# Optimization experiments

Measured on AMD Instinct MI355X. Metric: run time of the kernel, lower is better.

## Reference

```python
import jax, jax.numpy as jnp
import numpy as np

N_NODES = 100000
HIDDEN = 64
N_EDGES = 1600000


def _sage_conv(x, edge_index, Wl, Wr, b):
    # PyG SAGEConv (mean aggr): out_i = W_l @ mean_{j->i} x_j + W_r @ x_i + b
    src, dst = edge_index[0], edge_index[1]
    msg = x[src]                                      # [E, H] gather
    agg = jax.ops.segment_sum(msg, dst, num_segments=N_NODES)  # [N, H]
    deg = jax.ops.segment_sum(jnp.ones((msg.shape[0],), x.dtype), dst,
                              num_segments=N_NODES)
    agg = agg / jnp.maximum(deg, 1.0)[:, None]
    return agg @ Wl.T + x @ Wr.T + b


def setup_inputs() -> dict:
    key = jax.random.key(0)
    ks = jax.random.split(key, 8)
    s = 1.0 / np.sqrt(HIDDEN)
    return {
        "emb": jax.random.normal(ks[0], (N_NODES, HIDDEN), jnp.float32),
        "Wl1": jax.random.normal(ks[1], (HIDDEN, HIDDEN), jnp.float32) * s,
        "Wr1": jax.random.normal(ks[2], (HIDDEN, HIDDEN), jnp.float32) * s,
        "b1": jnp.zeros((HIDDEN,), jnp.float32),
        "Wl2": jax.random.normal(ks[3], (HIDDEN, HIDDEN), jnp.float32) * s,
        "Wr2": jax.random.normal(ks[4], (HIDDEN, HIDDEN), jnp.float32) * s,
        "b2": jnp.zeros((HIDDEN,), jnp.float32),
        "node_id": jnp.arange(N_NODES, dtype=jnp.int64 if jax.config.jax_enable_x64 else jnp.int32),
        "edge_index": jax.random.randint(ks[5], (2, N_EDGES), 0, N_NODES),
    }


def reference(emb, Wl1, Wr1, b1, Wl2, Wr2, b2, node_id, edge_index):
    # Embedding lookup
    x = emb[node_id]                                   # [N, H]
    # GNN: relu(conv1) -> conv2
    x = jax.nn.relu(_sage_conv(x, edge_index, Wl1, Wr1, b1))
    x = _sage_conv(x, edge_index, Wl2, Wr2, b2)
    # Classifier: per-edge dot product of endpoint features
    ef1 = x[edge_index[0]]                             # [E, H]
    ef2 = x[edge_index[1]]                             # [E, H]
    return (ef1 * ef2).sum(axis=-1)                    # [E]
```

## Files before the change

kernel.cpp:

```cpp
#include <hip/hip_runtime.h>

#define N_NODES 100000
#define HID 64
#define N_EDGES 1600000
#define NB 391
#define C_EPB 6400

typedef __attribute__((ext_vector_type(8))) short bf16x8;
typedef __attribute__((ext_vector_type(4))) float f32x4;

__device__ __forceinline__ unsigned short f2bf(float f) {
    unsigned u = __float_as_uint(f);
    u = (u + 0x7FFFu + ((u >> 16) & 1u)) >> 16;
    return (unsigned short)u;
}
__device__ __forceinline__ float bf2f(unsigned short h) {
    return __uint_as_float(((unsigned)h) << 16);
}
__device__ __forceinline__ float bflo(unsigned w) { return __uint_as_float(w << 16); }
__device__ __forceinline__ float bfhi(unsigned w) { return __uint_as_float(w & 0xFFFF0000u); }

__global__ void gather_bf16_kernel(const float* __restrict__ emb,
                                   const int* __restrict__ nid,
                                   unsigned short* __restrict__ xh) {
    int i = blockIdx.x * blockDim.x + threadIdx.x;
    const int total = N_NODES * (HID / 4);
    if (i >= total) return;
    int row = i >> 4;
    int c   = i & 15;
    int s   = nid[row];
    float4 v = reinterpret_cast<const float4*>(emb)[(size_t)s * 16 + c];
    uint2 p;
    p.x = (unsigned)f2bf(v.x) | ((unsigned)f2bf(v.y) << 16);
    p.y = (unsigned)f2bf(v.z) | ((unsigned)f2bf(v.w) << 16);
    reinterpret_cast<uint2*>(xh)[(size_t)row * 16 + c] = p;
}

__global__ void bucket_hist(const int* __restrict__ dst,
                            int* __restrict__ bhist) {
    __shared__ int h[NB];
    for (int i = threadIdx.x; i < NB; i += blockDim.x) h[i] = 0;
    __syncthreads();
    int nt = gridDim.x * blockDim.x;
    const int4* d4 = (const int4*)dst;
    for (int q = blockIdx.x * blockDim.x + threadIdx.x; q < N_EDGES / 4; q += nt) {
        int4 v = d4[q];
        atomicAdd(&h[v.x >> 8], 1);
        atomicAdd(&h[v.y >> 8], 1);
        atomicAdd(&h[v.z >> 8], 1);
        atomicAdd(&h[v.w >> 8], 1);
    }
    __syncthreads();
    for (int i = threadIdx.x; i < NB; i += blockDim.x)
        if (h[i]) atomicAdd(&bhist[i], h[i]);
}

__global__ void bucket_scan(const int* __restrict__ bhist,
                            int* __restrict__ boff,
                            int* __restrict__ bcursor) {
    __shared__ int s[512];
    int v = (threadIdx.x < NB) ? bhist[threadIdx.x] : 0;
    s[threadIdx.x] = v;
    __syncthreads();
    for (int off = 1; off < 512; off <<= 1) {
        int t = (threadIdx.x >= off) ? s[threadIdx.x - off] : 0;
        __syncthreads();
        s[threadIdx.x] += t;
        __syncthreads();
    }
    if (threadIdx.x < NB) {
        int ex = s[threadIdx.x] - v;
        boff[threadIdx.x] = ex;
        bcursor[threadIdx.x] = ex;
    }
}

__global__ void bucket_scatter(const int* __restrict__ src,
                               const int* __restrict__ dst,
                               int* __restrict__ bcursor,
                               int2* __restrict__ pairs) {
    __shared__ int h[NB];
    __shared__ int base[NB];
    for (int i = threadIdx.x; i < NB; i += blockDim.x) h[i] = 0;
    __syncthreads();
    int e0 = blockIdx.x * C_EPB;
    int e1 = e0 + C_EPB; if (e1 > N_EDGES) e1 = N_EDGES;
    for (int e = e0 + threadIdx.x; e < e1; e += blockDim.x)
        atomicAdd(&h[dst[e] >> 8], 1);
    __syncthreads();
    for (int i = threadIdx.x; i < NB; i += blockDim.x) {
        int c = h[i];
        base[i] = c ? atomicAdd(&bcursor[i], c) : 0;
    }
    __syncthreads();
    for (int i = threadIdx.x; i < NB; i += blockDim.x) h[i] = 0;
    __syncthreads();
    for (int e = e0 + threadIdx.x; e < e1; e += blockDim.x) {
        int d = dst[e];
        int b = d >> 8;
        int slot = base[b] + atomicAdd(&h[b], 1);
        pairs[slot] = make_int2(src[e], d);
    }
}

__global__ void bucket_csr(const int2* __restrict__ pairs,
                           const int* __restrict__ boff,
                           const int* __restrict__ bcursor,
                           int* __restrict__ row_start,
                           int* __restrict__ adj) {
    __shared__ int cnt[256];
    __shared__ int sc[256];
    int b = blockIdx.x;
    int node0 = b << 8;
    int p0 = boff[b];
    int p1 = bcursor[b];
    int t = threadIdx.x;
    cnt[t] = 0;
    __syncthreads();
    for (int p = p0 + t; p < p1; p += 256)
        atomicAdd(&cnt[pairs[p].y & 255], 1);
    __syncthreads();
    int v = cnt[t];
    sc[t] = v;
    __syncthreads();
    for (int off = 1; off < 256; off <<= 1) {
        int u = (t >= off) ? sc[t - off] : 0;
        __syncthreads();
        sc[t] += u;
        __syncthreads();
    }
    sc[t] = p0 + sc[t] - v;
    __syncthreads();
    int node = node0 + t;
    if (node <= N_NODES) row_start[node] = sc[t];
    __syncthreads();
    for (int p = p0 + t; p < p1; p += 256) {
        int2 pr = pairs[p];
        int slot = atomicAdd(&sc[pr.y & 255], 1);
        adj[slot] = pr.x;
    }
}

__global__ void agg_kernel(const int* __restrict__ row_start,
                           const int* __restrict__ adj,
                           const unsigned short* __restrict__ xh,
                           unsigned short* __restrict__ M) {
    int lane = threadIdx.x & 63;
    int slot = lane >> 4;
    int c    = lane & 15;
    int wpb = blockDim.x >> 6;
    int wid = blockIdx.x * wpb + (threadIdx.x >> 6);
    int stride = gridDim.x * wpb;
    const uint2* xw = (const uint2*)xh;
    uint2* Mw = (uint2*)M;
    for (int row = wid; row < N_NODES; row += stride) {
        int beg = row_start[row], end = row_start[row + 1];
        float a0 = 0.f, a1 = 0.f, a2 = 0.f, a3 = 0.f;
        int j = beg + slot;
        for (; j + 12 < end; j += 16) {
            int s0 = adj[j], s1 = adj[j + 4], s2 = adj[j + 8], s3 = adj[j + 12];
            uint2 v0 = xw[(size_t)s0 * 16 + c];
            uint2 v1 = xw[(size_t)s1 * 16 + c];
            uint2 v2 = xw[(size_t)s2 * 16 + c];
            uint2 v3 = xw[(size_t)s3 * 16 + c];
            a0 += bflo(v0.x) + bflo(v1.x) + bflo(v2.x) + bflo(v3.x);
            a1 += bfhi(v0.x) + bfhi(v1.x) + bfhi(v2.x) + bfhi(v3.x);
            a2 += bflo(v0.y) + bflo(v1.y) + bflo(v2.y) + bflo(v3.y);
            a3 += bfhi(v0.y) + bfhi(v1.y) + bfhi(v2.y) + bfhi(v3.y);
        }
        for (; j < end; j += 4) {
            uint2 v = xw[(size_t)adj[j] * 16 + c];
            a0 += bflo(v.x); a1 += bfhi(v.x);
            a2 += bflo(v.y); a3 += bfhi(v.y);
        }
        a0 += __shfl_xor(a0, 16); a0 += __shfl_xor(a0, 32);
        a1 += __shfl_xor(a1, 16); a1 += __shfl_xor(a1, 32);
        a2 += __shfl_xor(a2, 16); a2 += __shfl_xor(a2, 32);
        a3 += __shfl_xor(a3, 16); a3 += __shfl_xor(a3, 32);
        if (slot == 0) {
            float inv = 1.0f / fmaxf((float)(end - beg), 1.0f);
            uint2 p;
            p.x = (unsigned)f2bf(a0 * inv) | ((unsigned)f2bf(a1 * inv) << 16);
            p.y = (unsigned)f2bf(a2 * inv) | ((unsigned)f2bf(a3 * inv) << 16);
            Mw[(size_t)row * 16 + c] = p;
        }
    }
}

__global__ void gemm_kernel(const unsigned short* __restrict__ Am,
                            const unsigned short* __restrict__ As,
                            const float* __restrict__ Wl,
                            const float* __restrict__ Wr,
                            const float* __restrict__ bias,
                            unsigned short* __restrict__ H,
                            int relu) {
    int lane = threadIdx.x & 63;
    int m = lane & 15, quad = lane >> 4;

    bf16x8 wf[2][2][4];
    for (int mat = 0; mat < 2; ++mat) {
        const float* W = mat ? Wr : Wl;
        for (int ks = 0; ks < 2; ++ks)
            for (int ct = 0; ct < 4; ++ct) {
                const float* p = W + (ct * 16 + m) * HID + ks * 32 + quad * 8;
                bf16x8 f;
                #pragma unroll
                for (int j = 0; j < 8; ++j) f[j] = (short)f2bf(p[j]);
                wf[mat][ks][ct] = f;
            }
    }
    float bv[4];
    #pragma unroll
    for (int ct = 0; ct < 4; ++ct) bv[ct] = bias[ct * 16 + m];

    int wpb = blockDim.x >> 6;
    int wid = blockIdx.x * wpb + (threadIdx.x >> 6);
    int stride = gridDim.x * wpb;
    const int NT = N_NODES / 16;
    for (int t = wid; t < NT; t += stride) {
        f32x4 acc[4] = {{0,0,0,0},{0,0,0,0},{0,0,0,0},{0,0,0,0}};
        size_t rowbase = ((size_t)t * 16 + m) * HID;
        #pragma unroll
        for (int ks = 0; ks < 2; ++ks) {
            bf16x8 a0 = *(const bf16x8*)(Am + rowbase + ks * 32 + quad * 8);
            bf16x8 a1 = *(const bf16x8*)(As + rowbase + ks * 32 + quad * 8);
            #pragma unroll
            for (int ct = 0; ct < 4; ++ct) {
                acc[ct] = __builtin_amdgcn_mfma_f32_16x16x32_bf16(a0, wf[0][ks][ct], acc[ct], 0, 0, 0);
                acc[ct] = __builtin_amdgcn_mfma_f32_16x16x32_bf16(a1, wf[1][ks][ct], acc[ct], 0, 0, 0);
            }
        }
        #pragma unroll
        for (int ct = 0; ct < 4; ++ct) {
            #pragma unroll
            for (int r = 0; r < 4; ++r) {
                float v = acc[ct][r] + bv[ct];
                if (relu) v = fmaxf(v, 0.f);
                H[((size_t)t * 16 + quad * 4 + r) * HID + ct * 16 + m] = f2bf(v);
            }
        }
    }
}

__global__ void edge_dot_kernel(const int* __restrict__ src,
                                const int* __restrict__ dst,
                                const unsigned short* __restrict__ h,
                                float* __restrict__ out) {
    int t = blockIdx.x * blockDim.x + threadIdx.x;
    int g = t >> 3;
    int c = t & 7;
    int e0 = g * 2;
    if (e0 >= N_EDGES) return;
    int a0 = src[e0],     b0 = dst[e0];
    int a1 = src[e0 + 1], b1 = dst[e0 + 1];
    const uint4* h4 = reinterpret_cast<const uint4*>(h);
    uint4 va0 = h4[(size_t)a0 * 8 + c];
    uint4 vb0 = h4[(size_t)b0 * 8 + c];
    uint4 va1 = h4[(size_t)a1 * 8 + c];
    uint4 vb1 = h4[(size_t)b1 * 8 + c];
    float p0 = bflo(va0.x) * bflo(vb0.x) + bfhi(va0.x) * bfhi(vb0.x)
             + bflo(va0.y) * bflo(vb0.y) + bfhi(va0.y) * bfhi(vb0.y)
             + bflo(va0.z) * bflo(vb0.z) + bfhi(va0.z) * bfhi(vb0.z)
             + bflo(va0.w) * bflo(vb0.w) + bfhi(va0.w) * bfhi(vb0.w);
    float p1 = bflo(va1.x) * bflo(vb1.x) + bfhi(va1.x) * bfhi(vb1.x)
             + bflo(va1.y) * bflo(vb1.y) + bfhi(va1.y) * bfhi(vb1.y)
             + bflo(va1.z) * bflo(vb1.z) + bfhi(va1.z) * bfhi(vb1.z)
             + bflo(va1.w) * bflo(vb1.w) + bfhi(va1.w) * bfhi(vb1.w);
    p0 += __shfl_xor(p0, 1); p0 += __shfl_xor(p0, 2); p0 += __shfl_xor(p0, 4);
    p1 += __shfl_xor(p1, 1); p1 += __shfl_xor(p1, 2); p1 += __shfl_xor(p1, 4);
    if (c == 0) reinterpret_cast<float2*>(out)[g] = make_float2(p0, p1);
}

extern "C" void kernel_launch(void* const* d_in, const int* in_sizes, int n_in,
                              void* d_out, int out_size, void* d_ws, size_t ws_size,
                              hipStream_t stream) {
    const float* emb = (const float*)d_in[0];
    const float* Wl1 = (const float*)d_in[1];
    const float* Wr1 = (const float*)d_in[2];
    const float* b1  = (const float*)d_in[3];
    const float* Wl2 = (const float*)d_in[4];
    const float* Wr2 = (const float*)d_in[5];
    const float* b2  = (const float*)d_in[6];
    const int*   nid = (const int*)d_in[7];
    const int*   ei  = (const int*)d_in[8];
    const int* esrc = ei;
    const int* edst = ei + N_EDGES;
    float* out = (float*)d_out;

    const size_t NH = (size_t)N_NODES * HID;
    unsigned short* xh  = (unsigned short*)d_ws;
    unsigned short* h1h = xh + NH;
    unsigned short* h2h = h1h + NH;
    unsigned short* M   = h2h + NH;
    int* ib        = (int*)(M + NH);
    int* row_start = ib;
    int* adj       = ib + N_NODES + 64;
    int2* pairs    = (int2*)(adj + N_EDGES + 64);
    int* bhist     = (int*)(pairs + N_EDGES);
    int* boff      = bhist + NB + 1;
    int* bcursor   = boff + NB + 1;

    hipMemsetAsync(bhist, 0, NB * sizeof(int), stream);

    gather_bf16_kernel<<<(N_NODES * 16 + 255) / 256, 256, 0, stream>>>(emb, nid, xh);

    bucket_hist<<<256, 256, 0, stream>>>(edst, bhist);
    bucket_scan<<<1, 512, 0, stream>>>(bhist, boff, bcursor);
    bucket_scatter<<<(N_EDGES + C_EPB - 1) / C_EPB, 256, 0, stream>>>(esrc, edst, bcursor, pairs);
    bucket_csr<<<NB, 256, 0, stream>>>(pairs, boff, bcursor, row_start, adj);

    agg_kernel<<<2048, 256, 0, stream>>>(row_start, adj, xh, M);
    gemm_kernel<<<512, 256, 0, stream>>>(M, xh, Wl1, Wr1, b1, h1h, 1);

    agg_kernel<<<2048, 256, 0, stream>>>(row_start, adj, h1h, M);
    gemm_kernel<<<512, 256, 0, stream>>>(M, h1h, Wl2, Wr2, b2, h2h, 0);

    edge_dot_kernel<<<((size_t)(N_EDGES / 2) * 8 + 255) / 256, 256, 0, stream>>>(esrc, edst, h2h, out);
}
```

Measured before the change: 302.4 us.

## Compute edge dot products in CSR order and fuse gather with histogram

The edge-dot classifier now walks the destination-sorted CSR. Each destination row is loaded once and reused across all its incoming edges, and results are scattered to their original edge positions through a new eord array built during CSR construction. The embedding gather and the bucket histogram are merged into one launch to drop a kernel launch. The costs are an extra 6.4 MB index array with its writes, scattered 4-byte output stores, and edge ids packed into 24 bits of the pair word.

```diff
diff --git a/kernel.cpp b/kernel.cpp
--- a/kernel.cpp
+++ b/kernel.cpp
@@ -5,6 +5,7 @@
 #define N_EDGES 1600000
 #define NB 391
 #define C_EPB 6400
+#define GATHER_BLOCKS 6250
 
 typedef __attribute__((ext_vector_type(8))) short bf16x8;
 typedef __attribute__((ext_vector_type(4))) float f32x4;
@@ -20,30 +21,32 @@
 __device__ __forceinline__ float bflo(unsigned w) { return __uint_as_float(w << 16); }
 __device__ __forceinline__ float bfhi(unsigned w) { return __uint_as_float(w & 0xFFFF0000u); }
 
-__global__ void gather_bf16_kernel(const float* __restrict__ emb,
+__global__ void gather_hist_kernel(const float* __restrict__ emb,
                                    const int* __restrict__ nid,
-                                   unsigned short* __restrict__ xh) {
-    int i = blockIdx.x * blockDim.x + threadIdx.x;
-    const int total = N_NODES * (HID / 4);
-    if (i >= total) return;
-    int row = i >> 4;
-    int c   = i & 15;
-    int s   = nid[row];
-    float4 v = reinterpret_cast<const float4*>(emb)[(size_t)s * 16 + c];
-    uint2 p;
-    p.x = (unsigned)f2bf(v.x) | ((unsigned)f2bf(v.y) << 16);
-    p.y = (unsigned)f2bf(v.z) | ((unsigned)f2bf(v.w) << 16);
-    reinterpret_cast<uint2*>(xh)[(size_t)row * 16 + c] = p;
-}
-
-__global__ void bucket_hist(const int* __restrict__ dst,
-                            int* __restrict__ bhist) {
+                                   unsigned short* __restrict__ xh,
+                                   const int* __restrict__ dst,
+                                   int* __restrict__ bhist) {
+    if (blockIdx.x < GATHER_BLOCKS) {
+        int i = blockIdx.x * blockDim.x + threadIdx.x;
+        const int total = N_NODES * (HID / 4);
+        if (i >= total) return;
+        int row = i >> 4;
+        int c   = i & 15;
+        int s   = nid[row];
+        float4 v = reinterpret_cast<const float4*>(emb)[(size_t)s * 16 + c];
+        uint2 p;
+        p.x = (unsigned)f2bf(v.x) | ((unsigned)f2bf(v.y) << 16);
+        p.y = (unsigned)f2bf(v.z) | ((unsigned)f2bf(v.w) << 16);
+        reinterpret_cast<uint2*>(xh)[(size_t)row * 16 + c] = p;
+        return;
+    }
     __shared__ int h[NB];
     for (int i = threadIdx.x; i < NB; i += blockDim.x) h[i] = 0;
     __syncthreads();
-    int nt = gridDim.x * blockDim.x;
+    int hb = blockIdx.x - GATHER_BLOCKS;
+    const int nt = 256 * 256;
     const int4* d4 = (const int4*)dst;
-    for (int q = blockIdx.x * blockDim.x + threadIdx.x; q < N_EDGES / 4; q += nt) {
+    for (int q = hb * blockDim.x + threadIdx.x; q < N_EDGES / 4; q += nt) {
         int4 v = d4[q];
         atomicAdd(&h[v.x >> 8], 1);
         atomicAdd(&h[v.y >> 8], 1);
@@ -99,7 +102,7 @@
         int d = dst[e];
         int b = d >> 8;
         int slot = base[b] + atomicAdd(&h[b], 1);
-        pairs[slot] = make_int2(src[e], d);
+        pairs[slot] = make_int2(src[e], (d & 255) | (e << 8));
     }
 }
 
@@ -107,7 +110,8 @@
                            const int* __restrict__ boff,
                            const int* __restrict__ bcursor,
                            int* __restrict__ row_start,
-                           int* __restrict__ adj) {
+                           int* __restrict__ adj,
+                           int* __restrict__ eord) {
     __shared__ int cnt[256];
     __shared__ int sc[256];
     int b = blockIdx.x;
@@ -138,6 +142,7 @@
         int2 pr = pairs[p];
         int slot = atomicAdd(&sc[pr.y & 255], 1);
         adj[slot] = pr.x;
+        eord[slot] = (int)(((unsigned)pr.y) >> 8);
     }
 }
 
@@ -242,33 +247,52 @@
     }
 }
 
-__global__ void edge_dot_kernel(const int* __restrict__ src,
-                                const int* __restrict__ dst,
-                                const unsigned short* __restrict__ h,
-                                float* __restrict__ out) {
-    int t = blockIdx.x * blockDim.x + threadIdx.x;
-    int g = t >> 3;
-    int c = t & 7;
-    int e0 = g * 2;
-    if (e0 >= N_EDGES) return;
-    int a0 = src[e0],     b0 = dst[e0];
-    int a1 = src[e0 + 1], b1 = dst[e0 + 1];
-    const uint4* h4 = reinterpret_cast<const uint4*>(h);
-    uint4 va0 = h4[(size_t)a0 * 8 + c];
-    uint4 vb0 = h4[(size_t)b0 * 8 + c];
-    uint4 va1 = h4[(size_t)a1 * 8 + c];
-    uint4 vb1 = h4[(size_t)b1 * 8 + c];
-    float p0 = bflo(va0.x) * bflo(vb0.x) + bfhi(va0.x) * bfhi(vb0.x)
-             + bflo(va0.y) * bflo(vb0.y) + bfhi(va0.y) * bfhi(vb0.y)
-             + bflo(va0.z) * bflo(vb0.z) + bfhi(va0.z) * bfhi(vb0.z)
-             + bflo(va0.w) * bflo(vb0.w) + bfhi(va0.w) * bfhi(vb0.w);
-    float p1 = bflo(va1.x) * bflo(vb1.x) + bfhi(va1.x) * bfhi(vb1.x)
-             + bflo(va1.y) * bflo(vb1.y) + bfhi(va1.y) * bfhi(vb1.y)
-             + bflo(va1.z) * bflo(vb1.z) + bfhi(va1.z) * bfhi(vb1.z)
-             + bflo(va1.w) * bflo(vb1.w) + bfhi(va1.w) * bfhi(vb1.w);
-    p0 += __shfl_xor(p0, 1); p0 += __shfl_xor(p0, 2); p0 += __shfl_xor(p0, 4);
-    p1 += __shfl_xor(p1, 1); p1 += __shfl_xor(p1, 2); p1 += __shfl_xor(p1, 4);
-    if (c == 0) reinterpret_cast<float2*>(out)[g] = make_float2(p0, p1);
+__global__ void edge_dot_csr_kernel(const int* __restrict__ row_start,
+                                    const int* __restrict__ adj,
+                                    const int* __restrict__ eord,
+                                    const unsigned short* __restrict__ h,
+                                    float* __restrict__ out) {
+    int lane = threadIdx.x & 63;
+    int slot = lane >> 4;
+    int c    = lane & 15;
+    int wpb = blockDim.x >> 6;
+    int wid = blockIdx.x * wpb + (threadIdx.x >> 6);
+    int stride = gridDim.x * wpb;
+    const uint2* hw = (const uint2*)h;
+    for (int row = wid; row < N_NODES; row += stride) {
+        int beg = row_start[row], end = row_start[row + 1];
+        if (beg == end) continue;
+        uint2 vd = hw[(size_t)row * 16 + c];
+        float d0 = bflo(vd.x), d1 = bfhi(vd.x), d2 = bflo(vd.y), d3 = bfhi(vd.y);
+        int j = beg + slot;
+        for (; j + 12 < end; j += 16) {
+            int s0 = adj[j], s1 = adj[j + 4], s2 = adj[j + 8], s3 = adj[j + 12];
+            int e0 = eord[j], e1 = eord[j + 4], e2 = eord[j + 8], e3 = eord[j + 12];
+            uint2 v0 = hw[(size_t)s0 * 16 + c];
+            uint2 v1 = hw[(size_t)s1 * 16 + c];
+            uint2 v2 = hw[(size_t)s2 * 16 + c];
+            uint2 v3 = hw[(size_t)s3 * 16 + c];
+            float p0 = bflo(v0.x) * d0 + bfhi(v0.x) * d1 + bflo(v0.y) * d2 + bfhi(v0.y) * d3;
+            float p1 = bflo(v1.x) * d0 + bfhi(v1.x) * d1 + bflo(v1.y) * d2 + bfhi(v1.y) * d3;
+            float p2 = bflo(v2.x) * d0 + bfhi(v2.x) * d1 + bflo(v2.y) * d2 + bfhi(v2.y) * d3;
+            float p3 = bflo(v3.x) * d0 + bfhi(v3.x) * d1 + bflo(v3.y) * d2 + bfhi(v3.y) * d3;
+            p0 += __shfl_xor(p0, 1); p0 += __shfl_xor(p0, 2); p0 += __shfl_xor(p0, 4); p0 += __shfl_xor(p0, 8);
+            p1 += __shfl_xor(p1, 1); p1 += __shfl_xor(p1, 2); p1 += __shfl_xor(p1, 4); p1 += __shfl_xor(p1, 8);
+            p2 += __shfl_xor(p2, 1); p2 += __shfl_xor(p2, 2); p2 += __shfl_xor(p2, 4); p2 += __shfl_xor(p2, 8);
+            p3 += __shfl_xor(p3, 1); p3 += __shfl_xor(p3, 2); p3 += __shfl_xor(p3, 4); p3 += __shfl_xor(p3, 8);
+            if (c == 0) {
+                out[e0] = p0; out[e1] = p1; out[e2] = p2; out[e3] = p3;
+            }
+        }
+        for (; j < end; j += 4) {
+            int s = adj[j];
+            int e = eord[j];
+            uint2 v = hw[(size_t)s * 16 + c];
+            float p = bflo(v.x) * d0 + bfhi(v.x) * d1 + bflo(v.y) * d2 + bfhi(v.y) * d3;
+            p += __shfl_xor(p, 1); p += __shfl_xor(p, 2); p += __shfl_xor(p, 4); p += __shfl_xor(p, 8);
+            if (c == 0) out[e] = p;
+        }
+    }
 }
 
 extern "C" void kernel_launch(void* const* d_in, const int* in_sizes, int n_in,
@@ -295,19 +319,19 @@
     int* ib        = (int*)(M + NH);
     int* row_start = ib;
     int* adj       = ib + N_NODES + 64;
-    int2* pairs    = (int2*)(adj + N_EDGES + 64);
+    int* eord      = adj + N_EDGES;
+    int2* pairs    = (int2*)(eord + N_EDGES);
     int* bhist     = (int*)(pairs + N_EDGES);
     int* boff      = bhist + NB + 1;
     int* bcursor   = boff + NB + 1;
 
     hipMemsetAsync(bhist, 0, NB * sizeof(int), stream);
 
-    gather_bf16_kernel<<<(N_NODES * 16 + 255) / 256, 256, 0, stream>>>(emb, nid, xh);
-
-    bucket_hist<<<256, 256, 0, stream>>>(edst, bhist);
+    gather_hist_kernel<<<GATHER_BLOCKS + 256, 256, 0, stream>>>(emb, nid, xh, edst, bhist);
+
     bucket_scan<<<1, 512, 0, stream>>>(bhist, boff, bcursor);
     bucket_scatter<<<(N_EDGES + C_EPB - 1) / C_EPB, 256, 0, stream>>>(esrc, edst, bcursor, pairs);
-    bucket_csr<<<NB, 256, 0, stream>>>(pairs, boff, bcursor, row_start, adj);
+    bucket_csr<<<NB, 256, 0, stream>>>(pairs, boff, bcursor, row_start, adj, eord);
 
     agg_kernel<<<2048, 256, 0, stream>>>(row_start, adj, xh, M);
     gemm_kernel<<<512, 256, 0, stream>>>(M, xh, Wl1, Wr1, b1, h1h, 1);
@@ -315,5 +339,5 @@
     agg_kernel<<<2048, 256, 0, stream>>>(row_start, adj, h1h, M);
     gemm_kernel<<<512, 256, 0, stream>>>(M, h1h, Wl2, Wr2, b2, h2h, 0);
 
-    edge_dot_kernel<<<((size_t)(N_EDGES / 2) * 8 + 255) / 256, 256, 0, stream>>>(esrc, edst, h2h, out);
-}
+    edge_dot_csr_kernel<<<2048, 256, 0, stream>>>(row_start, adj, eord, h2h, out);
+}
```

Result: slower. 333.3 us (+10.2%).

## Fuse gather with bucket histogram and assign one row per 16-lane group in aggregation

Applied to the files above, without the earlier changes.

The embedding gather/bf16 conversion and the destination bucket histogram now run as one launch, with block index ranges selecting the role, which saves a kernel launch and lets the two independent jobs overlap. The aggregation kernel now has each 16-lane group of a wavefront handle its own destination row instead of splitting one row's neighbours across four slots. This removes the cross-slot shuffle reduction and increases the number of neighbour loads in flight (8 per iteration). The trade-off is that degree imbalance between the four rows sharing a wavefront can cause divergence, and the 8-wide unroll uses more registers.

```diff
diff --git a/kernel.cpp b/kernel.cpp
--- a/kernel.cpp
+++ b/kernel.cpp
@@ -5,6 +5,7 @@
 #define N_EDGES 1600000
 #define NB 391
 #define C_EPB 6400
+#define GATHER_BLOCKS 6250
 
 typedef __attribute__((ext_vector_type(8))) short bf16x8;
 typedef __attribute__((ext_vector_type(4))) float f32x4;
@@ -20,30 +21,32 @@
 __device__ __forceinline__ float bflo(unsigned w) { return __uint_as_float(w << 16); }
 __device__ __forceinline__ float bfhi(unsigned w) { return __uint_as_float(w & 0xFFFF0000u); }
 
-__global__ void gather_bf16_kernel(const float* __restrict__ emb,
+__global__ void gather_hist_kernel(const float* __restrict__ emb,
                                    const int* __restrict__ nid,
-                                   unsigned short* __restrict__ xh) {
-    int i = blockIdx.x * blockDim.x + threadIdx.x;
-    const int total = N_NODES * (HID / 4);
-    if (i >= total) return;
-    int row = i >> 4;
-    int c   = i & 15;
-    int s   = nid[row];
-    float4 v = reinterpret_cast<const float4*>(emb)[(size_t)s * 16 + c];
-    uint2 p;
-    p.x = (unsigned)f2bf(v.x) | ((unsigned)f2bf(v.y) << 16);
-    p.y = (unsigned)f2bf(v.z) | ((unsigned)f2bf(v.w) << 16);
-    reinterpret_cast<uint2*>(xh)[(size_t)row * 16 + c] = p;
-}
-
-__global__ void bucket_hist(const int* __restrict__ dst,
-                            int* __restrict__ bhist) {
+                                   unsigned short* __restrict__ xh,
+                                   const int* __restrict__ dst,
+                                   int* __restrict__ bhist) {
+    if (blockIdx.x < GATHER_BLOCKS) {
+        int i = blockIdx.x * blockDim.x + threadIdx.x;
+        const int total = N_NODES * (HID / 4);
+        if (i >= total) return;
+        int row = i >> 4;
+        int c   = i & 15;
+        int s   = nid[row];
+        float4 v = reinterpret_cast<const float4*>(emb)[(size_t)s * 16 + c];
+        uint2 p;
+        p.x = (unsigned)f2bf(v.x) | ((unsigned)f2bf(v.y) << 16);
+        p.y = (unsigned)f2bf(v.z) | ((unsigned)f2bf(v.w) << 16);
+        reinterpret_cast<uint2*>(xh)[(size_t)row * 16 + c] = p;
+        return;
+    }
     __shared__ int h[NB];
     for (int i = threadIdx.x; i < NB; i += blockDim.x) h[i] = 0;
     __syncthreads();
-    int nt = gridDim.x * blockDim.x;
+    int hb = blockIdx.x - GATHER_BLOCKS;
+    const int nt = 256 * 256;
     const int4* d4 = (const int4*)dst;
-    for (int q = blockIdx.x * blockDim.x + threadIdx.x; q < N_EDGES / 4; q += nt) {
+    for (int q = hb * blockDim.x + threadIdx.x; q < N_EDGES / 4; q += nt) {
         int4 v = d4[q];
         atomicAdd(&h[v.x >> 8], 1);
         atomicAdd(&h[v.y >> 8], 1);
@@ -146,19 +149,41 @@
                            const unsigned short* __restrict__ xh,
                            unsigned short* __restrict__ M) {
     int lane = threadIdx.x & 63;
-    int slot = lane >> 4;
-    int c    = lane & 15;
+    int g = lane >> 4;
+    int c = lane & 15;
     int wpb = blockDim.x >> 6;
     int wid = blockIdx.x * wpb + (threadIdx.x >> 6);
     int stride = gridDim.x * wpb;
     const uint2* xw = (const uint2*)xh;
     uint2* Mw = (uint2*)M;
-    for (int row = wid; row < N_NODES; row += stride) {
+    const int NQ = N_NODES / 4;
+    for (int q = wid; q < NQ; q += stride) {
+        int row = q * 4 + g;
         int beg = row_start[row], end = row_start[row + 1];
         float a0 = 0.f, a1 = 0.f, a2 = 0.f, a3 = 0.f;
-        int j = beg + slot;
-        for (; j + 12 < end; j += 16) {
-            int s0 = adj[j], s1 = adj[j + 4], s2 = adj[j + 8], s3 = adj[j + 12];
+        int j = beg;
+        for (; j + 7 < end; j += 8) {
+            int s0 = adj[j],     s1 = adj[j + 1], s2 = adj[j + 2], s3 = adj[j + 3];
+            int s4 = adj[j + 4], s5 = adj[j + 5], s6 = adj[j + 6], s7 = adj[j + 7];
+            uint2 v0 = xw[(size_t)s0 * 16 + c];
+            uint2 v1 = xw[(size_t)s1 * 16 + c];
+            uint2 v2 = xw[(size_t)s2 * 16 + c];
+            uint2 v3 = xw[(size_t)s3 * 16 + c];
+            uint2 v4 = xw[(size_t)s4 * 16 + c];
+            uint2 v5 = xw[(size_t)s5 * 16 + c];
+            uint2 v6 = xw[(size_t)s6 * 16 + c];
+            uint2 v7 = xw[(size_t)s7 * 16 + c];
+            a0 += bflo(v0.x) + bflo(v1.x) + bflo(v2.x) + bflo(v3.x)
+                + bflo(v4.x) + bflo(v5.x) + bflo(v6.x) + bflo(v7.x);
+            a1 += bfhi(v0.x) + bfhi(v1.x) + bfhi(v2.x) + bfhi(v3.x)
+                + bfhi(v4.x) + bfhi(v5.x) + bfhi(v6.x) + bfhi(v7.x);
+            a2 += bflo(v0.y) + bflo(v1.y) + bflo(v2.y) + bflo(v3.y)
+                + bflo(v4.y) + bflo(v5.y) + bflo(v6.y) + bflo(v7.y);
+            a3 += bfhi(v0.y) + bfhi(v1.y) + bfhi(v2.y) + bfhi(v3.y)
+                + bfhi(v4.y) + bfhi(v5.y) + bfhi(v6.y) + bfhi(v7.y);
+        }
+        if (j + 3 < end) {
+            int s0 = adj[j], s1 = adj[j + 1], s2 = adj[j + 2], s3 = adj[j + 3];
             uint2 v0 = xw[(size_t)s0 * 16 + c];
             uint2 v1 = xw[(size_t)s1 * 16 + c];
             uint2 v2 = xw[(size_t)s2 * 16 + c];
@@ -167,23 +192,18 @@
             a1 += bfhi(v0.x) + bfhi(v1.x) + bfhi(v2.x) + bfhi(v3.x);
             a2 += bflo(v0.y) + bflo(v1.y) + bflo(v2.y) + bflo(v3.y);
             a3 += bfhi(v0.y) + bfhi(v1.y) + bfhi(v2.y) + bfhi(v3.y);
-        }
-        for (; j < end; j += 4) {
+            j += 4;
+        }
+        for (; j < end; ++j) {
             uint2 v = xw[(size_t)adj[j] * 16 + c];
             a0 += bflo(v.x); a1 += bfhi(v.x);
             a2 += bflo(v.y); a3 += bfhi(v.y);
         }
-        a0 += __shfl_xor(a0, 16); a0 += __shfl_xor(a0, 32);
-        a1 += __shfl_xor(a1, 16); a1 += __shfl_xor(a1, 32);
-        a2 += __shfl_xor(a2, 16); a2 += __shfl_xor(a2, 32);
-        a3 += __shfl_xor(a3, 16); a3 += __shfl_xor(a3, 32);
-        if (slot == 0) {
-            float inv = 1.0f / fmaxf((float)(end - beg), 1.0f);
-            uint2 p;
-            p.x = (unsigned)f2bf(a0 * inv) | ((unsigned)f2bf(a1 * inv) << 16);
-            p.y = (unsigned)f2bf(a2 * inv) | ((unsigned)f2bf(a3 * inv) << 16);
-            Mw[(size_t)row * 16 + c] = p;
-        }
+        float inv = 1.0f / fmaxf((float)(end - beg), 1.0f);
+        uint2 p;
+        p.x = (unsigned)f2bf(a0 * inv) | ((unsigned)f2bf(a1 * inv) << 16);
+        p.y = (unsigned)f2bf(a2 * inv) | ((unsigned)f2bf(a3 * inv) << 16);
+        Mw[(size_t)row * 16 + c] = p;
     }
 }
 
@@ -302,9 +322,8 @@
 
     hipMemsetAsync(bhist, 0, NB * sizeof(int), stream);
 
-    gather_bf16_kernel<<<(N_NODES * 16 + 255) / 256, 256, 0, stream>>>(emb, nid, xh);
-
-    bucket_hist<<<256, 256, 0, stream>>>(edst, bhist);
+    gather_hist_kernel<<<GATHER_BLOCKS + 256, 256, 0, stream>>>(emb, nid, xh, edst, bhist);
+
     bucket_scan<<<1, 512, 0, stream>>>(bhist, boff, bcursor);
     bucket_scatter<<<(N_EDGES + C_EPB - 1) / C_EPB, 256, 0, stream>>>(esrc, edst, bcursor, pairs);
     bucket_csr<<<NB, 256, 0, stream>>>(pairs, boff, bcursor, row_start, adj);
```

Measured after the change: 283.9 us. -6.1%, faster.
